# Kernel optimization log

Measured on AMD Instinct MI355X. Metric: run time of the kernel, lower is better.

## Reference

```python
import jax, jax.numpy as jnp
import numpy as np

B, S, HID = 2, 2048, 2048
NH, NKV, DH = 16, 4, 128
EPS = 1e-6

def rotate_half(x):
    x1, x2 = x[..., : x.shape[-1] // 2], x[..., x.shape[-1] // 2 :]
    return jnp.concatenate((-x2, x1), axis=-1)

def rms_norm(x, w):
    var = jnp.mean(jnp.square(x), axis=-1, keepdims=True)
    return w * (x * jax.lax.rsqrt(var + EPS))

def setup_inputs() -> dict:
    key = jax.random.key(0)
    ks = jax.random.split(key, 8)
    hidden_states = jax.random.normal(ks[0], (B, S, HID), dtype=jnp.float32)
    # causal additive mask, broadcastable to [B, H, S, S]
    causal = jnp.tril(jnp.ones((S, S), dtype=bool))
    attention_mask = jnp.where(causal, 0.0, -1e9).astype(jnp.float32)[None, None]
    # RoPE tables: [1, S, 1, DH] to broadcast over (B, S, H, DH)
    inv_freq = 1.0 / (10000.0 ** (np.arange(0, DH, 2, dtype=np.float32) / DH))
    t = np.arange(S, dtype=np.float32)
    freqs = np.einsum('s,d->sd', t, inv_freq)
    emb = np.concatenate([freqs, freqs], axis=-1)  # [S, DH]
    cos = jnp.asarray(np.cos(emb))[None, :, None, :]
    sin = jnp.asarray(np.sin(emb))[None, :, None, :]
    std = 0.02
    Wq = jax.random.normal(ks[1], (HID, NH * DH), dtype=jnp.float32) * std
    Wk = jax.random.normal(ks[2], (HID, NKV * DH), dtype=jnp.float32) * std
    Wv = jax.random.normal(ks[3], (HID, NKV * DH), dtype=jnp.float32) * std
    Wo = jax.random.normal(ks[4], (NH * DH, HID), dtype=jnp.float32) * std
    q_norm_w = jnp.ones((DH,), dtype=jnp.float32)
    k_norm_w = jnp.ones((DH,), dtype=jnp.float32)
    return dict(hidden_states=hidden_states, attention_mask=attention_mask,
                cos=cos, sin=sin, Wq=Wq, Wk=Wk, Wv=Wv, Wo=Wo,
                q_norm_w=q_norm_w, k_norm_w=k_norm_w)

def reference(hidden_states, attention_mask, cos, sin, Wq, Wk, Wv, Wo, q_norm_w, k_norm_w):
    b, s, _ = hidden_states.shape
    q = (hidden_states @ Wq).reshape(b, s, NH, DH)
    k = (hidden_states @ Wk).reshape(b, s, NKV, DH)
    v = (hidden_states @ Wv).reshape(b, s, NKV, DH)
    # per-head RMSNorm on q/k
    q = rms_norm(q, q_norm_w)
    k = rms_norm(k, k_norm_w)
    # RoPE
    q = q * cos + rotate_half(q) * sin
    k = k * cos + rotate_half(k) * sin
    # GQA: repeat kv heads
    groups = NH // NKV
    k = jnp.repeat(k, groups, axis=2)
    v = jnp.repeat(v, groups, axis=2)
    scale = 1.0 / jnp.sqrt(jnp.asarray(DH, dtype=q.dtype))
    scores = jnp.einsum('bqhd,bkhd->bhqk', q, k) * scale  # [B,H,S,S]
    scores = scores + attention_mask
    probs = jax.nn.softmax(scores, axis=-1)
    out = jnp.einsum('bhqk,bkhd->bqhd', probs, v)
    out = out.reshape(b, s, NH * DH)
    return out @ Wo
```

## Files before the change

kernel.cpp:

```cpp
#include <hip/hip_runtime.h>
#include <hip/hip_bf16.h>
#include <stdint.h>


typedef __attribute__((ext_vector_type(8))) short short8;
typedef __attribute__((ext_vector_type(4))) float floatx4;
typedef __hip_bfloat16 bf16_t;

#define MFMA16x16(a, b, c) __builtin_amdgcn_mfma_f32_16x16x32_bf16(a, b, c, 0, 0, 0)

__device__ __forceinline__ void async_copy16(const void* g, void* l) {
  __builtin_amdgcn_global_load_lds(
      (const __attribute__((address_space(1))) void*)g,
      (__attribute__((address_space(3))) void*)l, 16, 0, 0);
}

__device__ __forceinline__ unsigned short bf16bits(float x) {
  bf16_t h = __float2bfloat16(x);
  return *reinterpret_cast<unsigned short*>(&h);
}

__global__ __launch_bounds__(256) void convbf_kernel(const float* __restrict__ in,
                                                     bf16_t* __restrict__ out, int n4) {
  int i = blockIdx.x * 256 + threadIdx.x;
  if (i < n4) {
    const float4 v = reinterpret_cast<const float4*>(in)[i];
    ushort4 o;
    o.x = bf16bits(v.x); o.y = bf16bits(v.y); o.z = bf16bits(v.z); o.w = bf16bits(v.w);
    reinterpret_cast<ushort4*>(out)[i] = o;
  }
}

__global__ __launch_bounds__(256) void wtrans_kernel(const float* __restrict__ W,
                                                     bf16_t* __restrict__ Wt, int N, int roff) {
  __shared__ float t[32][33];
  int k0 = blockIdx.y * 32, n0 = blockIdx.x * 32;
#pragma unroll
  for (int j = 0; j < 4; ++j)
    t[threadIdx.y + j * 8][threadIdx.x] =
        W[(size_t)(k0 + threadIdx.y + j * 8) * N + n0 + threadIdx.x];
  __syncthreads();
#pragma unroll
  for (int j = 0; j < 4; ++j) {
    int n = n0 + threadIdx.y + j * 8, k = k0 + threadIdx.x;
    Wt[(size_t)(roff + n) * 2048 + k] = __float2bfloat16(t[threadIdx.x][threadIdx.y + j * 8]);
  }
}

template <int OBF>
__global__ __launch_bounds__(256, 3) void gemm_bt_kernel(const bf16_t* __restrict__ A,
                                                         const bf16_t* __restrict__ Bt,
                                                         void* __restrict__ Cv,
                                                         int K, int ldc) {
  __shared__ __align__(16) char smem[32768];
  const int tid = threadIdx.x;
  const int wave = tid >> 6, lane = tid & 63;
  const int wr = wave >> 1, wc = wave & 1;
  const int l16 = lane & 15, lhi = lane >> 4;

  const int nwg = gridDim.x * gridDim.y;
  const int orig = blockIdx.y * gridDim.x + blockIdx.x;
  const int swz = (orig & 7) * (nwg >> 3) + (orig >> 3);
  const int bn = (swz % gridDim.x) * 128;
  const int bm = (swz / gridDim.x) * 128;

  floatx4 acc[4][4] = {};

  for (int k0 = 0; k0 < K; k0 += 64) {
    __syncthreads();
#pragma unroll
    for (int i = 0; i < 4; ++i) {
      int chunk = i * 4 + wave;
      unsigned p = (unsigned)chunk * 1024u + (unsigned)lane * 16u;
      unsigned row = p >> 7;
      unsigned colg = (p & 127u) ^ ((row & 7u) << 4);
      const char* gA = (const char*)(A + (size_t)(bm + row) * K + k0) + colg;
      async_copy16(gA, smem + (size_t)chunk * 1024);
      const char* gB = (const char*)(Bt + (size_t)(bn + row) * K + k0) + colg;
      async_copy16(gB, smem + 16384 + (size_t)chunk * 1024);
    }
    __syncthreads();
#pragma unroll
    for (int kk = 0; kk < 2; ++kk) {
      short8 fa[4], fb[4];
#pragma unroll
      for (int mi = 0; mi < 4; ++mi) {
        unsigned row = wr * 64 + mi * 16 + l16;
        unsigned off = row * 128u + kk * 64u + lhi * 16u;
        off ^= (row & 7u) << 4;
        fa[mi] = *(const short8*)(smem + off);
      }
#pragma unroll
      for (int ni = 0; ni < 4; ++ni) {
        unsigned row = wc * 64 + ni * 16 + l16;
        unsigned off = row * 128u + kk * 64u + lhi * 16u;
        off ^= (row & 7u) << 4;
        fb[ni] = *(const short8*)(smem + 16384 + off);
      }
#pragma unroll
      for (int mi = 0; mi < 4; ++mi)
#pragma unroll
        for (int ni = 0; ni < 4; ++ni)
          acc[mi][ni] = MFMA16x16(fa[mi], fb[ni], acc[mi][ni]);
    }
  }
#pragma unroll
  for (int mi = 0; mi < 4; ++mi)
#pragma unroll
    for (int ni = 0; ni < 4; ++ni)
#pragma unroll
      for (int r = 0; r < 4; ++r) {
        int row = bm + wr * 64 + mi * 16 + lhi * 4 + r;
        int col = bn + wc * 64 + ni * 16 + l16;
        if (OBF)
          ((bf16_t*)Cv)[(size_t)row * ldc + col] = __float2bfloat16(acc[mi][ni][r]);
        else
          ((float*)Cv)[(size_t)row * ldc + col] = acc[mi][ni][r];
      }
}

__global__ __launch_bounds__(256) void qknorm_rope_kernel(
    const bf16_t* __restrict__ Cqkv, const float* __restrict__ cosT,
    const float* __restrict__ sinT, const float* __restrict__ qw,
    const float* __restrict__ kw, bf16_t* __restrict__ Qa, bf16_t* __restrict__ Ka) {
  int wave = threadIdx.x >> 6, lane = threadIdx.x & 63;
  int task = blockIdx.x * 4 + wave;
  int unit = task % 20;
  int row = task / 20;
  int b = row >> 11, s = row & 2047;
  const bf16_t* src;
  const float* w;
  bf16_t* dst;
  float sc;
  if (unit < 16) {
    src = Cqkv + (size_t)row * 3072 + unit * 128;
    w = qw;
    dst = Qa + ((size_t)(b * 16 + unit) * 2048 + s) * 128;
    sc = 0.088388347648318447f;
  } else {
    int kh = unit - 16;
    src = Cqkv + (size_t)row * 3072 + 2048 + kh * 128;
    w = kw;
    dst = Ka + ((size_t)(b * 4 + kh) * 2048 + s) * 128;
    sc = 1.0f;
  }
  float x1 = __bfloat162float(src[lane]), x2 = __bfloat162float(src[lane + 64]);
  float ss = x1 * x1 + x2 * x2;
#pragma unroll
  for (int off = 1; off < 64; off <<= 1) ss += __shfl_xor(ss, off, 64);
  float inv = rsqrtf(ss * (1.f / 128.f) + 1e-6f);
  x1 = x1 * inv * w[lane];
  x2 = x2 * inv * w[lane + 64];
  float c1 = cosT[(size_t)s * 128 + lane], c2 = cosT[(size_t)s * 128 + lane + 64];
  float s1 = sinT[(size_t)s * 128 + lane], s2 = sinT[(size_t)s * 128 + lane + 64];
  dst[lane] = __float2bfloat16((x1 * c1 - x2 * s1) * sc);
  dst[lane + 64] = __float2bfloat16((x2 * c2 + x1 * s2) * sc);
}

__global__ __launch_bounds__(256) void vtrans_kernel(const bf16_t* __restrict__ Cqkv,
                                                     bf16_t* __restrict__ Vt) {
  __shared__ bf16_t t[32][33];
  int bk = blockIdx.z;
  int b = bk >> 2, kh = bk & 3;
  int s0 = blockIdx.x * 32, d0 = blockIdx.y * 32;
  const bf16_t* src = Cqkv + (size_t)(b * 2048) * 3072 + 2560 + kh * 128;
#pragma unroll
  for (int j = 0; j < 4; ++j)
    t[threadIdx.y + j * 8][threadIdx.x] =
        src[(size_t)(s0 + threadIdx.y + j * 8) * 3072 + d0 + threadIdx.x];
  __syncthreads();
  bf16_t* dst = Vt + (size_t)(b * 4 + kh) * 128 * 2048;
#pragma unroll
  for (int j = 0; j < 4; ++j) {
    int d = d0 + threadIdx.y + j * 8, s = s0 + threadIdx.x;
    dst[(size_t)d * 2048 + s] = t[threadIdx.x][threadIdx.y + j * 8];
  }
}

__device__ __forceinline__ unsigned swz_row(unsigned row) {
  return (((row & 7u) ^ ((row >> 3) << 1)) & 7u) << 4;
}

__global__ __launch_bounds__(256, 2) void flash_kernel(const bf16_t* __restrict__ Qa,
                                                       const bf16_t* __restrict__ Ka,
                                                       const bf16_t* __restrict__ Vt,
                                                       bf16_t* __restrict__ attnO) {
  __shared__ __align__(16) char smem[65536];
  const int tid = threadIdx.x;
  const int wave = tid >> 6, lane = tid & 63;
  const int l16 = lane & 15, lhi = lane >> 4;
  const int bid = blockIdx.x;
  const int bh = bid & 31;
  const int ib = bid >> 5;
  const int qb = (ib < 8) ? (15 - ib) : (ib - 8);
  const int h = bh & 15, b = bh >> 4;
  const int kh = h >> 2;
  const int q0b = qb << 7;
  const int q0w = q0b + wave * 32;

  const bf16_t* Qb = Qa + ((size_t)bh * 2048 + q0w) * 128;
  const bf16_t* Kb = Ka + (size_t)(b * 4 + kh) * 2048 * 128;
  const bf16_t* Vb = Vt + (size_t)(b * 4 + kh) * 128 * 2048;

  short8 qf[2][4];
#pragma unroll
  for (int rt = 0; rt < 2; ++rt)
#pragma unroll
    for (int kk = 0; kk < 4; ++kk)
      qf[rt][kk] = *(const short8*)(Qb + (size_t)(rt * 16 + l16) * 128 + kk * 32 + lhi * 8);

  short8 onesf;
#pragma unroll
  for (int j = 0; j < 8; ++j) onesf[j] = (short)0x3F80;

  floatx4 o[2][8] = {};
  floatx4 lsum[2] = {};
  short8 pf[2][2];
  float m[2] = {-1e30f, -1e30f};

  const float THR = 8.0f;
  const int nch = 2 * qb + 2;

  auto stageK = [&](int key0, char* dstK) {
#pragma unroll
    for (int it = 0; it < 4; ++it) {
      unsigned p = (unsigned)(it * 4 + wave) * 1024u + (unsigned)lane * 16u;
      unsigned row = p >> 8;
      unsigned gcol = (p & 255u) ^ swz_row(row);
      async_copy16((const char*)(Kb + (size_t)(key0 + row) * 128) + gcol,
                   dstK + (size_t)(it * 4 + wave) * 1024);
    }
  };
  auto stageV = [&](int key0, char* dstV) {
#pragma unroll
    for (int it = 0; it < 4; ++it) {
      unsigned p = (unsigned)(it * 4 + wave) * 1024u + (unsigned)lane * 16u;
      unsigned row = p >> 7;
      unsigned gcol = (p & 127u) ^ swz_row(row);
      async_copy16((const char*)(Vb + (size_t)row * 2048 + key0) + gcol,
                   dstV + (size_t)(it * 4 + wave) * 1024);
    }
  };

  stageK(0, smem);
  stageV(0, smem + 16384);

  int cur = 0;
  for (int c = 0; c < nch; ++c) {
    const int kc0 = c << 6;
    const bool active = (kc0 <= q0w + 31);
    char* Kl = smem + (size_t)cur * 32768;
    char* Vl = Kl + 16384;
    char* Kn = smem + (size_t)(cur ^ 1) * 32768;

    if (c + 1 < nch) {
      stageK(kc0 + 64, Kn);
      stageV(kc0 + 64, Kn + 16384);
      asm volatile("s_waitcnt vmcnt(8)" ::: "memory");
    } else {
      asm volatile("s_waitcnt vmcnt(0)" ::: "memory");
    }
    __builtin_amdgcn_s_barrier();
    __builtin_amdgcn_sched_barrier(0);

    if (active) {
      floatx4 s[2][4] = {};
      __builtin_amdgcn_s_setprio(1);
#pragma unroll
      for (int g = 0; g < 4; ++g) {
        unsigned row = (unsigned)(l16 >> 2) * 8u + (unsigned)((g & 1) * 4) +
                       (unsigned)(l16 & 3) + (unsigned)((g >> 1) * 32);
        unsigned base = row * 256u;
        unsigned px = swz_row(row);
#pragma unroll
        for (int kk = 0; kk < 4; ++kk) {
          short8 kf = *(const short8*)(Kl + base + (((unsigned)(kk * 64 + lhi * 16)) ^ px));
          s[0][g] = MFMA16x16(kf, qf[0][kk], s[0][g]);
          s[1][g] = MFMA16x16(kf, qf[1][kk], s[1][g]);
        }
      }
      __builtin_amdgcn_s_setprio(0);

      const bool needMask = (kc0 + 64 > q0w);
#pragma unroll
      for (int rt = 0; rt < 2; ++rt) {
        const int qrow = q0w + rt * 16 + l16;
        if (needMask) {
#pragma unroll
          for (int g = 0; g < 4; ++g)
#pragma unroll
            for (int r = 0; r < 4; ++r) {
              int key = kc0 + lhi * 8 + (g & 1) * 4 + r + (g >> 1) * 32;
              if (key > qrow) s[rt][g][r] = -1e9f;
            }
        }
        float mx = s[rt][0][0];
#pragma unroll
        for (int g = 0; g < 4; ++g)
#pragma unroll
          for (int r = 0; r < 4; ++r) mx = fmaxf(mx, s[rt][g][r]);
        mx = fmaxf(mx, __shfl_xor(mx, 16, 64));
        mx = fmaxf(mx, __shfl_xor(mx, 32, 64));
        bool grow = mx > m[rt] + THR;
        if (__any(grow)) {
          float mn = fmaxf(m[rt], mx);
          float corr = __expf(m[rt] - mn);
          m[rt] = mn;
#pragma unroll
          for (int r = 0; r < 4; ++r) {
            float co = __shfl(corr, lhi * 4 + r, 64);
            lsum[rt][r] *= co;
#pragma unroll
            for (int f = 0; f < 8; ++f) o[rt][f][r] *= co;
          }
        }
#pragma unroll
        for (int ks = 0; ks < 2; ++ks) {
          union { unsigned u[4]; short8 v; } pk;
#pragma unroll
          for (int half = 0; half < 2; ++half) {
            int g = ks * 2 + half;
            float p0 = __expf(s[rt][g][0] - m[rt]);
            float p1 = __expf(s[rt][g][1] - m[rt]);
            float p2 = __expf(s[rt][g][2] - m[rt]);
            float p3 = __expf(s[rt][g][3] - m[rt]);
            pk.u[half * 2] = (unsigned)bf16bits(p0) | ((unsigned)bf16bits(p1) << 16);
            pk.u[half * 2 + 1] = (unsigned)bf16bits(p2) | ((unsigned)bf16bits(p3) << 16);
          }
          pf[rt][ks] = pk.v;
        }
      }

      __builtin_amdgcn_s_setprio(1);
#pragma unroll
      for (int ks = 0; ks < 2; ++ks) {
#pragma unroll
        for (int f = 0; f < 8; ++f) {
          unsigned row = (unsigned)(f * 16 + l16);
          short8 vf = *(const short8*)(Vl + row * 128u +
                                       (((unsigned)(ks * 64 + lhi * 16)) ^ swz_row(row)));
          o[0][f] = MFMA16x16(pf[0][ks], vf, o[0][f]);
          o[1][f] = MFMA16x16(pf[1][ks], vf, o[1][f]);
        }
        lsum[0] = MFMA16x16(pf[0][ks], onesf, lsum[0]);
        lsum[1] = MFMA16x16(pf[1][ks], onesf, lsum[1]);
      }
      __builtin_amdgcn_s_setprio(0);
    }

    __builtin_amdgcn_s_barrier();
    cur ^= 1;
  }

#pragma unroll
  for (int rt = 0; rt < 2; ++rt)
#pragma unroll
    for (int r = 0; r < 4; ++r) {
      float inv = 1.f / lsum[rt][r];
      int row = q0w + rt * 16 + lhi * 4 + r;
      size_t base = ((size_t)(b * 2048) + row) * 2048 + h * 128;
#pragma unroll
      for (int f = 0; f < 8; ++f)
        attnO[base + f * 16 + l16] = __float2bfloat16(o[rt][f][r] * inv);
    }
}

extern "C" void kernel_launch(void* const* d_in, const int* in_sizes, int n_in,
                              void* d_out, int out_size, void* d_ws, size_t ws_size,
                              hipStream_t stream) {
  const float* hs = (const float*)d_in[0];
  const float* cosT = (const float*)d_in[2];
  const float* sinT = (const float*)d_in[3];
  const float* Wq = (const float*)d_in[4];
  const float* Wk = (const float*)d_in[5];
  const float* Wv = (const float*)d_in[6];
  const float* Wo = (const float*)d_in[7];
  const float* qw = (const float*)d_in[8];
  const float* kw = (const float*)d_in[9];
  float* out = (float*)d_out;

  char* ws = (char*)d_ws;
  size_t off = 0;
  auto alloc = [&](size_t bytes) {
    char* p = ws + off;
    off += (bytes + 255) & ~(size_t)255;
    return p;
  };
  bf16_t* hsb  = (bf16_t*)alloc((size_t)4096 * 2048 * 2);
  bf16_t* wqkv = (bf16_t*)alloc((size_t)3072 * 2048 * 2);
  bf16_t* wot  = (bf16_t*)alloc((size_t)2048 * 2048 * 2);
  bf16_t* cqkv = (bf16_t*)alloc((size_t)4096 * 3072 * 2);
  bf16_t* qa   = (bf16_t*)alloc((size_t)2 * 16 * 2048 * 128 * 2);
  bf16_t* ka   = (bf16_t*)alloc((size_t)2 * 4 * 2048 * 128 * 2);
  bf16_t* vt   = (bf16_t*)alloc((size_t)2 * 4 * 2048 * 128 * 2);
  bf16_t* attn = (bf16_t*)cqkv;

  convbf_kernel<<<8192, 256, 0, stream>>>(hs, hsb, 2097152);
  dim3 tb(32, 8);
  wtrans_kernel<<<dim3(64, 64), tb, 0, stream>>>(Wq, wqkv, 2048, 0);
  wtrans_kernel<<<dim3(16, 64), tb, 0, stream>>>(Wk, wqkv, 512, 2048);
  wtrans_kernel<<<dim3(16, 64), tb, 0, stream>>>(Wv, wqkv, 512, 2560);
  wtrans_kernel<<<dim3(64, 64), tb, 0, stream>>>(Wo, wot, 2048, 0);
  gemm_bt_kernel<1><<<dim3(24, 32), 256, 0, stream>>>(hsb, wqkv, cqkv, 2048, 3072);
  qknorm_rope_kernel<<<20480, 256, 0, stream>>>(cqkv, cosT, sinT, qw, kw, qa, ka);
  vtrans_kernel<<<dim3(64, 4, 8), tb, 0, stream>>>(cqkv, vt);
  flash_kernel<<<512, 256, 0, stream>>>(qa, ka, vt, attn);
  gemm_bt_kernel<0><<<dim3(16, 32), 256, 0, stream>>>(attn, wot, out, 2048, 2048);
}
```

Before: 203.1 us.

## Use 128-key chunks with single-buffered K/V and staggered async staging

The attention kernel now processes 128 keys per iteration instead of 64, with single K and V buffers in LDS instead of double-buffered 64-key tiles. The next K tile is loaded while P·V runs, and the next V tile is loaded after P·V finishes. The goal is to halve loop iterations and barriers and to raise MFMA work per chunk. In exchange, the per-wave active-chunk skip is dropped, more causally masked work is done near the diagonal, and more accumulator registers are live. There is also no explicit wait for outstanding async loads before the LDS reads, only __syncthreads.

New measurement: 216.5 us. 6.6% more time.

```diff
diff --git a/kernel.cpp b/kernel.cpp
--- a/kernel.cpp
+++ b/kernel.cpp
@@ -202,6 +202,9 @@
   const bf16_t* Kb = Ka + (size_t)(b * 4 + kh) * 2048 * 128;
   const bf16_t* Vb = Vt + (size_t)(b * 4 + kh) * 128 * 2048;
 
+  char* Kl = smem;
+  char* Vl = smem + 32768;
+
   short8 qf[2][4];
 #pragma unroll
   for (int rt = 0; rt < 2; ++rt)
@@ -215,141 +218,130 @@
 
   floatx4 o[2][8] = {};
   floatx4 lsum[2] = {};
-  short8 pf[2][2];
+  short8 pf[2][4];
   float m[2] = {-1e30f, -1e30f};
 
   const float THR = 8.0f;
-  const int nch = 2 * qb + 2;
-
-  auto stageK = [&](int key0, char* dstK) {
-#pragma unroll
-    for (int it = 0; it < 4; ++it) {
+  const int nch = qb + 1;
+
+  auto stageK = [&](int key0) {
+#pragma unroll
+    for (int it = 0; it < 8; ++it) {
       unsigned p = (unsigned)(it * 4 + wave) * 1024u + (unsigned)lane * 16u;
       unsigned row = p >> 8;
       unsigned gcol = (p & 255u) ^ swz_row(row);
       async_copy16((const char*)(Kb + (size_t)(key0 + row) * 128) + gcol,
-                   dstK + (size_t)(it * 4 + wave) * 1024);
+                   Kl + (size_t)(it * 4 + wave) * 1024);
     }
   };
-  auto stageV = [&](int key0, char* dstV) {
-#pragma unroll
-    for (int it = 0; it < 4; ++it) {
+  auto stageV = [&](int key0) {
+#pragma unroll
+    for (int it = 0; it < 8; ++it) {
       unsigned p = (unsigned)(it * 4 + wave) * 1024u + (unsigned)lane * 16u;
-      unsigned row = p >> 7;
-      unsigned gcol = (p & 127u) ^ swz_row(row);
+      unsigned row = p >> 8;
+      unsigned gcol = (p & 255u) ^ swz_row(row);
       async_copy16((const char*)(Vb + (size_t)row * 2048 + key0) + gcol,
-                   dstV + (size_t)(it * 4 + wave) * 1024);
+                   Vl + (size_t)(it * 4 + wave) * 1024);
     }
   };
 
-  stageK(0, smem);
-  stageV(0, smem + 16384);
-
-  int cur = 0;
+  stageK(0);
+  stageV(0);
+  __syncthreads();
+
   for (int c = 0; c < nch; ++c) {
-    const int kc0 = c << 6;
-    const bool active = (kc0 <= q0w + 31);
-    char* Kl = smem + (size_t)cur * 32768;
-    char* Vl = Kl + 16384;
-    char* Kn = smem + (size_t)(cur ^ 1) * 32768;
-
-    if (c + 1 < nch) {
-      stageK(kc0 + 64, Kn);
-      stageV(kc0 + 64, Kn + 16384);
-      asm volatile("s_waitcnt vmcnt(8)" ::: "memory");
-    } else {
-      asm volatile("s_waitcnt vmcnt(0)" ::: "memory");
-    }
-    __builtin_amdgcn_s_barrier();
-    __builtin_amdgcn_sched_barrier(0);
-
-    if (active) {
-      floatx4 s[2][4] = {};
-      __builtin_amdgcn_s_setprio(1);
-#pragma unroll
-      for (int g = 0; g < 4; ++g) {
-        unsigned row = (unsigned)(l16 >> 2) * 8u + (unsigned)((g & 1) * 4) +
-                       (unsigned)(l16 & 3) + (unsigned)((g >> 1) * 32);
-        unsigned base = row * 256u;
-        unsigned px = swz_row(row);
-#pragma unroll
-        for (int kk = 0; kk < 4; ++kk) {
-          short8 kf = *(const short8*)(Kl + base + (((unsigned)(kk * 64 + lhi * 16)) ^ px));
-          s[0][g] = MFMA16x16(kf, qf[0][kk], s[0][g]);
-          s[1][g] = MFMA16x16(kf, qf[1][kk], s[1][g]);
+    const int kc0 = c << 7;
+
+    floatx4 s[2][8] = {};
+    __builtin_amdgcn_s_setprio(1);
+#pragma unroll
+    for (int g = 0; g < 8; ++g) {
+      unsigned row = (unsigned)(l16 >> 2) * 8u + (unsigned)((g & 1) * 4) +
+                     (unsigned)(l16 & 3) + (unsigned)((g >> 1) * 32);
+      unsigned base = row * 256u;
+      unsigned px = swz_row(row);
+#pragma unroll
+      for (int kk = 0; kk < 4; ++kk) {
+        short8 kf = *(const short8*)(Kl + base + (((unsigned)(kk * 64 + lhi * 16)) ^ px));
+        s[0][g] = MFMA16x16(kf, qf[0][kk], s[0][g]);
+        s[1][g] = MFMA16x16(kf, qf[1][kk], s[1][g]);
+      }
+    }
+    __builtin_amdgcn_s_setprio(0);
+
+    const bool needMask = (kc0 + 128 > q0w);
+#pragma unroll
+    for (int rt = 0; rt < 2; ++rt) {
+      const int qrow = q0w + rt * 16 + l16;
+      if (needMask) {
+#pragma unroll
+        for (int g = 0; g < 8; ++g)
+#pragma unroll
+          for (int r = 0; r < 4; ++r) {
+            int key = kc0 + lhi * 8 + (g & 1) * 4 + r + (g >> 1) * 32;
+            if (key > qrow) s[rt][g][r] = -1e9f;
+          }
+      }
+      float mx = s[rt][0][0];
+#pragma unroll
+      for (int g = 0; g < 8; ++g)
+#pragma unroll
+        for (int r = 0; r < 4; ++r) mx = fmaxf(mx, s[rt][g][r]);
+      mx = fmaxf(mx, __shfl_xor(mx, 16, 64));
+      mx = fmaxf(mx, __shfl_xor(mx, 32, 64));
+      bool grow = mx > m[rt] + THR;
+      if (__any(grow)) {
+        float mn = fmaxf(m[rt], mx);
+        float corr = __expf(m[rt] - mn);
+        m[rt] = mn;
+#pragma unroll
+        for (int r = 0; r < 4; ++r) {
+          float co = __shfl(corr, lhi * 4 + r, 64);
+          lsum[rt][r] *= co;
+#pragma unroll
+          for (int f = 0; f < 8; ++f) o[rt][f][r] *= co;
         }
       }
-      __builtin_amdgcn_s_setprio(0);
-
-      const bool needMask = (kc0 + 64 > q0w);
-#pragma unroll
-      for (int rt = 0; rt < 2; ++rt) {
-        const int qrow = q0w + rt * 16 + l16;
-        if (needMask) {
-#pragma unroll
-          for (int g = 0; g < 4; ++g)
-#pragma unroll
-            for (int r = 0; r < 4; ++r) {
-              int key = kc0 + lhi * 8 + (g & 1) * 4 + r + (g >> 1) * 32;
-              if (key > qrow) s[rt][g][r] = -1e9f;
-            }
+#pragma unroll
+      for (int ks = 0; ks < 4; ++ks) {
+        union { unsigned u[4]; short8 v; } pk;
+#pragma unroll
+        for (int half = 0; half < 2; ++half) {
+          int g = ks * 2 + half;
+          float p0 = __expf(s[rt][g][0] - m[rt]);
+          float p1 = __expf(s[rt][g][1] - m[rt]);
+          float p2 = __expf(s[rt][g][2] - m[rt]);
+          float p3 = __expf(s[rt][g][3] - m[rt]);
+          pk.u[half * 2] = (unsigned)bf16bits(p0) | ((unsigned)bf16bits(p1) << 16);
+          pk.u[half * 2 + 1] = (unsigned)bf16bits(p2) | ((unsigned)bf16bits(p3) << 16);
         }
-        float mx = s[rt][0][0];
-#pragma unroll
-        for (int g = 0; g < 4; ++g)
-#pragma unroll
-          for (int r = 0; r < 4; ++r) mx = fmaxf(mx, s[rt][g][r]);
-        mx = fmaxf(mx, __shfl_xor(mx, 16, 64));
-        mx = fmaxf(mx, __shfl_xor(mx, 32, 64));
-        bool grow = mx > m[rt] + THR;
-        if (__any(grow)) {
-          float mn = fmaxf(m[rt], mx);
-          float corr = __expf(m[rt] - mn);
-          m[rt] = mn;
-#pragma unroll
-          for (int r = 0; r < 4; ++r) {
-            float co = __shfl(corr, lhi * 4 + r, 64);
-            lsum[rt][r] *= co;
-#pragma unroll
-            for (int f = 0; f < 8; ++f) o[rt][f][r] *= co;
-          }
-        }
-#pragma unroll
-        for (int ks = 0; ks < 2; ++ks) {
-          union { unsigned u[4]; short8 v; } pk;
-#pragma unroll
-          for (int half = 0; half < 2; ++half) {
-            int g = ks * 2 + half;
-            float p0 = __expf(s[rt][g][0] - m[rt]);
-            float p1 = __expf(s[rt][g][1] - m[rt]);
-            float p2 = __expf(s[rt][g][2] - m[rt]);
-            float p3 = __expf(s[rt][g][3] - m[rt]);
-            pk.u[half * 2] = (unsigned)bf16bits(p0) | ((unsigned)bf16bits(p1) << 16);
-            pk.u[half * 2 + 1] = (unsigned)bf16bits(p2) | ((unsigned)bf16bits(p3) << 16);
-          }
-          pf[rt][ks] = pk.v;
-        }
-      }
-
-      __builtin_amdgcn_s_setprio(1);
-#pragma unroll
-      for (int ks = 0; ks < 2; ++ks) {
-#pragma unroll
-        for (int f = 0; f < 8; ++f) {
-          unsigned row = (unsigned)(f * 16 + l16);
-          short8 vf = *(const short8*)(Vl + row * 128u +
-                                       (((unsigned)(ks * 64 + lhi * 16)) ^ swz_row(row)));
-          o[0][f] = MFMA16x16(pf[0][ks], vf, o[0][f]);
-          o[1][f] = MFMA16x16(pf[1][ks], vf, o[1][f]);
-        }
-        lsum[0] = MFMA16x16(pf[0][ks], onesf, lsum[0]);
-        lsum[1] = MFMA16x16(pf[1][ks], onesf, lsum[1]);
-      }
-      __builtin_amdgcn_s_setprio(0);
-    }
-
-    __builtin_amdgcn_s_barrier();
-    cur ^= 1;
+        pf[rt][ks] = pk.v;
+      }
+    }
+
+    __syncthreads();
+
+    if (c + 1 < nch) stageK(kc0 + 128);
+
+    __builtin_amdgcn_s_setprio(1);
+#pragma unroll
+    for (int ks = 0; ks < 4; ++ks) {
+#pragma unroll
+      for (int f = 0; f < 8; ++f) {
+        unsigned row = (unsigned)(f * 16 + l16);
+        short8 vf = *(const short8*)(Vl + row * 256u +
+                                     (((unsigned)(ks * 64 + lhi * 16)) ^ swz_row(row)));
+        o[0][f] = MFMA16x16(pf[0][ks], vf, o[0][f]);
+        o[1][f] = MFMA16x16(pf[1][ks], vf, o[1][f]);
+      }
+      lsum[0] = MFMA16x16(pf[0][ks], onesf, lsum[0]);
+      lsum[1] = MFMA16x16(pf[1][ks], onesf, lsum[1]);
+    }
+    __builtin_amdgcn_s_setprio(0);
+
+    __syncthreads();
+
+    if (c + 1 < nch) stageV(kc0 + 128);
   }
 
 #pragma unroll
```
